# Kernel tuning notes

Hardware: AMD Instinct MI355X
Metric: run time of the kernel (lower is better)

Reference implementation:

```python
import jax, jax.numpy as jnp
from jax import lax
import numpy as np

GRID = 8
H384 = 6 * GRID * GRID  # 384, LSTM input and hidden size


def _conv(x, w, b):
    # x: [B,C,H,W], w: [O,I,kh,kw]
    y = lax.conv_general_dilated(x, w, (1, 1), 'VALID',
                                 dimension_numbers=('NCHW', 'OIHW', 'NCHW'))
    return y + b[None, :, None, None]


def _maxpool2(x):
    return lax.reduce_window(x, -jnp.inf, lax.max,
                             (1, 1, 2, 2), (1, 1, 2, 2), 'VALID')


def setup_inputs() -> dict:
    key = jax.random.key(0)
    ks = jax.random.split(key, 20)
    s = 0.05
    d = {
        'x': jax.random.normal(ks[0], (512, 100, 100), jnp.float32),
        # conv stack: Conv2d(1,16,7) ... Conv2d(128,128,3)
        'cw1': jax.random.normal(ks[1], (16, 1, 7, 7), jnp.float32) * s,
        'cb1': jnp.zeros((16,), jnp.float32),
        'cw2': jax.random.normal(ks[2], (32, 16, 4, 4), jnp.float32) * s,
        'cb2': jnp.zeros((32,), jnp.float32),
        'cw3': jax.random.normal(ks[3], (64, 32, 5, 5), jnp.float32) * s,
        'cb3': jnp.zeros((64,), jnp.float32),
        'cw4': jax.random.normal(ks[4], (128, 64, 5, 5), jnp.float32) * s,
        'cb4': jnp.zeros((128,), jnp.float32),
        'cw5': jax.random.normal(ks[5], (128, 128, 5, 5), jnp.float32) * s,
        'cb5': jnp.zeros((128,), jnp.float32),
        'cw6': jax.random.normal(ks[6], (128, 128, 3, 3), jnp.float32) * s,
        'cb6': jnp.zeros((128,), jnp.float32),
        # linear layers: 8192 -> 1024 -> 384, Sigmoid
        'lw1': jax.random.normal(ks[7], (1024, 8192), jnp.float32) * 0.01,
        'lb1': jnp.zeros((1024,), jnp.float32),
        'lw2': jax.random.normal(ks[8], (384, 1024), jnp.float32) * 0.02,
        'lb2': jnp.zeros((384,), jnp.float32),
        # LSTM (input 384, hidden 384, 1 layer), torch gate order i,f,g,o
        'w_ih': jax.random.normal(ks[9], (4 * H384, H384), jnp.float32) * s,
        'w_hh': jax.random.normal(ks[10], (4 * H384, H384), jnp.float32) * s,
        'b_ih': jnp.zeros((4 * H384,), jnp.float32),
        'b_hh': jnp.zeros((4 * H384,), jnp.float32),
    }
    return d


def reference(x, cw1, cb1, cw2, cb2, cw3, cb3, cw4, cb4, cw5, cb5, cw6, cb6,
              lw1, lb1, lw2, lb2, w_ih, w_hh, b_ih, b_hh):
    B = x.shape[0]
    h = x[:, None, :, :]                       # [B,1,100,100]
    h = _maxpool2(jax.nn.relu(_conv(h, cw1, cb1)))   # [B,16,47,47]
    h = _maxpool2(jax.nn.relu(_conv(h, cw2, cb2)))   # [B,32,22,22]
    h = jax.nn.relu(_conv(h, cw3, cb3))              # [B,64,18,18]
    h = jax.nn.relu(_conv(h, cw4, cb4))              # [B,128,14,14]
    h = jax.nn.relu(_conv(h, cw5, cb5))              # [B,128,10,10]
    h = jax.nn.relu(_conv(h, cw6, cb6))              # [B,128,8,8]
    h = h.reshape(B, -1)                             # [B,8192]
    h = h @ lw1.T + lb1                              # [B,1024]
    h = jax.nn.sigmoid(h @ lw2.T + lb2)              # [B,384]

    # Sequential LSTM over the batch dim with carried (h,c) state
    def step(carry, xt):
        hs, cs = carry
        gates = w_ih @ xt + b_ih + w_hh @ hs + b_hh  # [1536]
        i, f, g, o = jnp.split(gates, 4)
        cs = jax.nn.sigmoid(f) * cs + jax.nn.sigmoid(i) * jnp.tanh(g)
        hs = jax.nn.sigmoid(o) * jnp.tanh(cs)
        return (hs, cs), hs

    init = (jnp.zeros((H384,), x.dtype), jnp.zeros((H384,), x.dtype))
    _, ys = lax.scan(step, init, h)                  # [B,384]
    return ys.reshape(B, 6, GRID, GRID)
```

## Files before the change

### kernel.cpp

```cpp
#include <hip/hip_runtime.h>
#include <cstddef>
#include <cstdint>

#define T256 256

typedef __attribute__((ext_vector_type(8))) short bhalf8;
typedef __attribute__((ext_vector_type(4))) float floatx4;

__device__ __forceinline__ ushort f2bf(float f) {
  union { float f; uint32_t u; } v; v.f = f;
  return (ushort)((v.u + 0x7fffu + ((v.u >> 16) & 1u)) >> 16);
}

__global__ __launch_bounds__(256) void conv1_pool_k(
    const float* __restrict__ x, const float* __restrict__ w,
    const float* __restrict__ bias, float* __restrict__ out)
{
  __shared__ float img[10000];
  __shared__ float wsm[16 * 49];
  __shared__ float bsm[16];
  const int b = blockIdx.x, tid = threadIdx.x;
  for (int i = tid; i < 10000; i += T256) img[i] = x[(size_t)b * 10000 + i];
  for (int i = tid; i < 16 * 49; i += T256) wsm[i] = w[i];
  if (tid < 16) bsm[tid] = bias[tid];
  __syncthreads();
  for (int p = tid; p < 47 * 47; p += T256) {
    const int py = p / 47, px = p % 47;
    const int iy0 = 2 * py, ix0 = 2 * px;
    float win[8][8];
#pragma unroll
    for (int r = 0; r < 8; ++r)
#pragma unroll
      for (int c = 0; c < 8; ++c)
        win[r][c] = img[(iy0 + r) * 100 + (ix0 + c)];
#pragma unroll 2
    for (int oc = 0; oc < 16; ++oc) {
      float m = 0.f;
#pragma unroll
      for (int dy = 0; dy < 2; ++dy)
#pragma unroll
        for (int dx = 0; dx < 2; ++dx) {
          float s = bsm[oc];
#pragma unroll
          for (int ky = 0; ky < 7; ++ky)
#pragma unroll
            for (int kx = 0; kx < 7; ++kx)
              s += win[dy + ky][dx + kx] * wsm[oc * 49 + ky * 7 + kx];
          m = fmaxf(m, s);
        }
      out[((size_t)b * 16 + oc) * 2209 + p] = m;
    }
  }
}

__global__ __launch_bounds__(256) void wprep_k(
    const float* __restrict__ w, ushort* __restrict__ bswz,
    int IC, int KW, int OC, int total)
{
  const int idx = blockIdx.x * 256 + threadIdx.x;
  if (idx >= total) return;
  const int NT = OC / 16;
  const int lane = idx & 63;
  const int nt = (idx >> 6) % NT;
  const int ks = idx / (64 * NT);
  const int oc = nt * 16 + (lane & 15);
  const int kb = ks * 32 + (lane >> 4) * 8;
  ushort tmp[8];
#pragma unroll
  for (int j = 0; j < 8; ++j) {
    const int k = kb + j;
    const int ic = k % IC, tap = k / IC;
    tmp[j] = f2bf(w[((size_t)oc * IC + ic) * (KW * KW) + tap]);
  }
  *(bhalf8*)(bswz + (size_t)idx * 8) = *(const bhalf8*)tmp;
}

__global__ __launch_bounds__(256) void wprep_lin_k(
    const float* __restrict__ w, ushort* __restrict__ bswz,
    int Kdim, int NT, int total)
{
  const int idx = blockIdx.x * 256 + threadIdx.x;
  if (idx >= total) return;
  const int lane = idx & 63;
  const int nt = (idx >> 6) % NT;
  const int ks = idx / (64 * NT);
  const int oc = nt * 16 + (lane & 15);
  const int kb = ks * 32 + (lane >> 4) * 8;
  ushort tmp[8];
#pragma unroll
  for (int j = 0; j < 8; ++j) tmp[j] = f2bf(w[(size_t)oc * Kdim + kb + j]);
  *(bhalf8*)(bswz + (size_t)idx * 8) = *(const bhalf8*)tmp;
}

__global__ __launch_bounds__(256) void f2bf_k(
    const float* __restrict__ in, ushort* __restrict__ outv, int n)
{
  const int i = (blockIdx.x * 256 + threadIdx.x) * 4;
  if (i >= n) return;
  const float4 v = *(const float4*)&in[i];
  ushort tmp[4] = {f2bf(v.x), f2bf(v.y), f2bf(v.z), f2bf(v.w)};
  *(uint2*)&outv[i] = *(const uint2*)tmp;
}

__global__ __launch_bounds__(256) void conv2mfma_k(
    const float* __restrict__ in, const ushort* __restrict__ bswz,
    const float* __restrict__ bias, float* __restrict__ out)
{
  constexpr int IC = 16, IH = 47, IW = 47;
  constexpr int NPIX = IH * IW;
  constexpr int ROWU = IC + 8;
  constexpr int KS = 8;
  __shared__ ushort imgT[NPIX * ROWU];
  const int b = blockIdx.x, tid = threadIdx.x;
  const int lane = tid & 63, wv = tid >> 6;

  for (int e = tid; e < IC * NPIX; e += 256) {
    const int ic = e / NPIX, pix = e % NPIX;
    imgT[pix * ROWU + ic] = f2bf(in[((size_t)b * IC + ic) * NPIX + pix]);
  }
  __syncthreads();

  const int col = lane & 15, g = lane >> 4;
  const float b0 = bias[col], b1 = bias[16 + col];

  for (int it = wv; it < 66; it += 4) {
    const int pyp = it / 3, tx = it - pyp * 3;
    int px = tx * 16 + col; px = px < 43 ? px : 43;
    floatx4 acc[2][2];
#pragma unroll
    for (int dy = 0; dy < 2; ++dy)
#pragma unroll
      for (int nt = 0; nt < 2; ++nt) acc[dy][nt] = (floatx4){0.f, 0.f, 0.f, 0.f};

    for (int ks = 0; ks < KS; ++ks) {
      bhalf8 bf[2];
#pragma unroll
      for (int nt = 0; nt < 2; ++nt)
        bf[nt] = *(const bhalf8*)(bswz + ((size_t)(ks * 2 + nt) * 64 + lane) * 8);
      const int kk = ks * 32 + g * 8;
      const int tap = kk >> 4, icb = kk & 15;
      const int ky = tap >> 2, kx = tap & 3;
      bhalf8 af[2];
#pragma unroll
      for (int dy = 0; dy < 2; ++dy)
        af[dy] = *(const bhalf8*)&imgT[((2 * pyp + dy + ky) * IW + px + kx) * ROWU + icb];
#pragma unroll
      for (int dy = 0; dy < 2; ++dy)
#pragma unroll
        for (int nt = 0; nt < 2; ++nt)
          acc[dy][nt] = __builtin_amdgcn_mfma_f32_16x16x32_bf16(
              af[dy], bf[nt], acc[dy][nt], 0, 0, 0);
    }
#pragma unroll
    for (int nt = 0; nt < 2; ++nt) {
      const int oc = nt * 16 + col;
      const float bb = nt ? b1 : b0;
      float vv[4];
#pragma unroll
      for (int i = 0; i < 4; ++i) vv[i] = fmaxf(acc[0][nt][i], acc[1][nt][i]);
#pragma unroll
      for (int q = 0; q < 2; ++q) {
        const int pxp = tx * 8 + g * 2 + q;
        if (pxp < 22) {
          const float v = fmaxf(fmaxf(vv[2 * q], vv[2 * q + 1]) + bb, 0.f);
          out[((size_t)b * 32 + oc) * 484 + pyp * 22 + pxp] = v;
        }
      }
    }
  }
}

template <int IC, int IH, int IW, int KW_, int OC, int MC>
__global__ __launch_bounds__(256) void convmfma_k(
    const float* __restrict__ in, const ushort* __restrict__ bswz,
    const float* __restrict__ bias, float* __restrict__ out)
{
  constexpr int OH = IH - KW_ + 1, OW = IW - KW_ + 1, P = OH * OW;
  constexpr int NPIX = IH * IW;
  constexpr int KS = IC * KW_ * KW_ / 32;
  constexpr int NT = OC / 16;
  constexpr int NPW = NT / 4;
  constexpr int MT = (P + 15) / 16;
  constexpr int ROWU = IC + 8;
  static_assert(NT % 4 == 0 && IC % 32 == 0, "cfg");

  __shared__ ushort imgT[NPIX * ROWU];
  const int b = blockIdx.x, tid = threadIdx.x;
  const int lane = tid & 63, wv = tid >> 6;
  const int icoff = (lane >> 4) * 8;

  for (int e = tid; e < IC * NPIX; e += 256) {
    const int ic = e / NPIX, pix = e % NPIX;
    imgT[pix * ROWU + ic] = f2bf(in[((size_t)b * IC + ic) * NPIX + pix]);
  }
  __syncthreads();

  for (int m0 = 0; m0 < MT; m0 += MC) {
    floatx4 acc[MC][NPW];
#pragma unroll
    for (int mi = 0; mi < MC; ++mi)
#pragma unroll
      for (int nn = 0; nn < NPW; ++nn)
        acc[mi][nn] = (floatx4){0.f, 0.f, 0.f, 0.f};

    int pbase[MC];
#pragma unroll
    for (int mi = 0; mi < MC; ++mi) {
      int p = (m0 + mi) * 16 + (lane & 15);
      p = p < P ? p : P - 1;
      pbase[mi] = ((p / OW) * IW + (p % OW)) * ROWU;
    }

    bhalf8 bcur[NPW];
#pragma unroll
    for (int nn = 0; nn < NPW; ++nn)
      bcur[nn] = *(const bhalf8*)(bswz + ((size_t)(wv * NPW + nn) * 64 + lane) * 8);

    for (int ks = 0; ks < KS; ++ks) {
      bhalf8 bnext[NPW];
      if (ks + 1 < KS) {
#pragma unroll
        for (int nn = 0; nn < NPW; ++nn)
          bnext[nn] = *(const bhalf8*)(bswz +
              ((size_t)((ks + 1) * NT + wv * NPW + nn) * 64 + lane) * 8);
      }
      const int tap = (ks * 32) / IC;
      const int icb = (ks * 32) % IC;
      const int aoff = ((tap / KW_) * IW + (tap % KW_)) * ROWU + icb + icoff;
      bhalf8 af[MC];
#pragma unroll
      for (int mi = 0; mi < MC; ++mi)
        af[mi] = *(const bhalf8*)&imgT[pbase[mi] + aoff];
#pragma unroll
      for (int mi = 0; mi < MC; ++mi)
#pragma unroll
        for (int nn = 0; nn < NPW; ++nn)
          acc[mi][nn] = __builtin_amdgcn_mfma_f32_16x16x32_bf16(
              af[mi], bcur[nn], acc[mi][nn], 0, 0, 0);
      if (ks + 1 < KS) {
#pragma unroll
        for (int nn = 0; nn < NPW; ++nn) bcur[nn] = bnext[nn];
      }
    }
#pragma unroll
    for (int mi = 0; mi < MC; ++mi)
#pragma unroll
      for (int nn = 0; nn < NPW; ++nn) {
        const int oc = (wv * NPW + nn) * 16 + (lane & 15);
#pragma unroll
        for (int i = 0; i < 4; ++i) {
          const int p = (m0 + mi) * 16 + (lane >> 4) * 4 + i;
          if (p < P) {
            const float v = fmaxf(acc[mi][nn][i] + bias[oc], 0.f);
            out[((size_t)b * OC + oc) * P + p] = v;
          }
        }
      }
  }
}

__global__ __launch_bounds__(256) void gemm_bf16_k(
    const ushort* __restrict__ abf, const ushort* __restrict__ bswz,
    const float* __restrict__ bias, float* __restrict__ C,
    int M, int N, int K)
{
  __shared__ ushort As[64][72];
  const int bn = blockIdx.x, bm = blockIdx.y, tid = threadIdx.x;
  const int lane = tid & 63, wv = tid >> 6;
  const int m0 = bm * 64, n0 = bn * 64;
  const int NTg = N / 16;
  const int ntg = bn * 4 + wv;
  floatx4 acc[4];
#pragma unroll
  for (int mt = 0; mt < 4; ++mt) acc[mt] = (floatx4){0.f, 0.f, 0.f, 0.f};

  for (int kc = 0; kc < K / 64; ++kc) {
    __syncthreads();
#pragma unroll
    for (int q = 0; q < 2; ++q) {
      const int id = q * 256 + tid;
      const int row = id >> 3, kcol = (id & 7) * 8;
      *(bhalf8*)&As[row][kcol] =
          *(const bhalf8*)&abf[(size_t)(m0 + row) * K + kc * 64 + kcol];
    }
    __syncthreads();
#pragma unroll
    for (int k2 = 0; k2 < 2; ++k2) {
      const int ks = kc * 2 + k2;
      const bhalf8 bf = *(const bhalf8*)(bswz + ((size_t)(ks * NTg + ntg) * 64 + lane) * 8);
      const int ksub = k2 * 32 + (lane >> 4) * 8;
#pragma unroll
      for (int mt = 0; mt < 4; ++mt) {
        const bhalf8 af = *(const bhalf8*)&As[mt * 16 + (lane & 15)][ksub];
        acc[mt] = __builtin_amdgcn_mfma_f32_16x16x32_bf16(af, bf, acc[mt], 0, 0, 0);
      }
    }
  }
  const int n = n0 + wv * 16 + (lane & 15);
  const float bb = bias[n];
#pragma unroll
  for (int mt = 0; mt < 4; ++mt)
#pragma unroll
    for (int i = 0; i < 4; ++i) {
      const int m = m0 + mt * 16 + (lane >> 4) * 4 + i;
      C[(size_t)m * N + n] = acc[mt][i] + bb;
    }
}

template <int ACT>
__global__ __launch_bounds__(256) void gemm_tn_k(
    const float* __restrict__ A, const float* __restrict__ B,
    const float* __restrict__ b1, const float* __restrict__ b2,
    float* __restrict__ C, int M, int N, int K)
{
  __shared__ float As[32][66];
  __shared__ float Bs[32][36];
  const int bn = blockIdx.x, bm = blockIdx.y, tid = threadIdx.x;
  const int tx = tid & 7, ty = tid >> 3;
  const int m0 = bm * 64, n0 = bn * 32;
  double acc[2][4] = {{0, 0, 0, 0}, {0, 0, 0, 0}};
  for (int k0 = 0; k0 < K; k0 += 32) {
    __syncthreads();
#pragma unroll
    for (int l = 0; l < 8; ++l) {
      int id = tid + l * 256;
      int kk = id & 31, mm = id >> 5;
      As[kk][mm] = A[(size_t)(m0 + mm) * K + (k0 + kk)];
    }
#pragma unroll
    for (int l = 0; l < 4; ++l) {
      int id = tid + l * 256;
      int kk = id & 31, nn = id >> 5;
      Bs[kk][nn] = B[(size_t)(n0 + nn) * K + (k0 + kk)];
    }
    __syncthreads();
    float p[2][4] = {{0.f, 0.f, 0.f, 0.f}, {0.f, 0.f, 0.f, 0.f}};
#pragma unroll
    for (int kk = 0; kk < 32; ++kk) {
      const float2 av = *reinterpret_cast<const float2*>(&As[kk][ty * 2]);
      const float4 bv = *reinterpret_cast<const float4*>(&Bs[kk][tx * 4]);
      p[0][0] += av.x * bv.x; p[0][1] += av.x * bv.y;
      p[0][2] += av.x * bv.z; p[0][3] += av.x * bv.w;
      p[1][0] += av.y * bv.x; p[1][1] += av.y * bv.y;
      p[1][2] += av.y * bv.z; p[1][3] += av.y * bv.w;
    }
#pragma unroll
    for (int i = 0; i < 2; ++i)
#pragma unroll
      for (int j = 0; j < 4; ++j) acc[i][j] += (double)p[i][j];
  }
#pragma unroll
  for (int i = 0; i < 2; ++i) {
    const int m = m0 + ty * 2 + i;
#pragma unroll
    for (int j = 0; j < 4; ++j) {
      const int n = n0 + tx * 4 + j;
      double v = acc[i][j] + (double)b1[n];
      if (b2) v += (double)b2[n];
      if (ACT == 1) v = 1.0 / (1.0 + exp(-v));
      C[(size_t)m * N + n] = (float)v;
    }
  }
}

#define NWG 16
#define CPW 24
__global__ __launch_bounds__(768) void lstm_k(
    const float* __restrict__ gin, const float* __restrict__ whh,
    float* __restrict__ out, unsigned long long* __restrict__ tagged)
{
  __shared__ __align__(16) float hsm[8][52];
  __shared__ float gsum[96];
  const int wg = blockIdx.x, tid = threadIdx.x;
  const int r = tid >> 3, lk = tid & 7;
  const int gq = r / CPW, cl = r % CPW;
  const int grow = gq * 384 + wg * CPW + cl;
  float wreg[48];
  {
    const float* wr = whh + (size_t)grow * 384 + lk * 48;
#pragma unroll
    for (int i = 0; i < 48; ++i) wreg[i] = wr[i];
  }
  float c = 0.f;
  __syncthreads();
  for (int t = 0; t < 512; ++t) {
    float g0 = 0.f, g1 = 0.f, g2 = 0.f, g3 = 0.f;
    if (tid < CPW) {
      const int j = wg * CPW + tid;
      g0 = gin[(size_t)t * 1536 + 0 * 384 + j];
      g1 = gin[(size_t)t * 1536 + 1 * 384 + j];
      g2 = gin[(size_t)t * 1536 + 2 * 384 + j];
      g3 = gin[(size_t)t * 1536 + 3 * 384 + j];
    }
    if (tid < 384) {
      float hv;
      if (t == 0) {
        hv = 0.f;
      } else {
        unsigned long long u;
        do {
          u = __hip_atomic_load(&tagged[(size_t)(t - 1) * 384 + tid],
                                __ATOMIC_RELAXED, __HIP_MEMORY_SCOPE_AGENT);
        } while ((unsigned)(u >> 32) != (unsigned)t);
        union { unsigned ui; float f; } cv; cv.ui = (unsigned)u; hv = cv.f;
      }
      hsm[tid / 48][tid % 48] = hv;
    }
    __syncthreads();
    float s = 0.f;
    {
      const float4* hp = (const float4*)&hsm[lk][0];
#pragma unroll
      for (int q = 0; q < 12; ++q) {
        const float4 hv = hp[q];
        s += wreg[4 * q + 0] * hv.x + wreg[4 * q + 1] * hv.y
           + wreg[4 * q + 2] * hv.z + wreg[4 * q + 3] * hv.w;
      }
    }
    s += __shfl_xor(s, 1);
    s += __shfl_xor(s, 2);
    s += __shfl_xor(s, 4);
    if (lk == 0) gsum[r] = s;
    __syncthreads();
    if (tid < CPW) {
      const float gi = gsum[0 * CPW + tid] + g0;
      const float gf = gsum[1 * CPW + tid] + g1;
      const float gg = gsum[2 * CPW + tid] + g2;
      const float go = gsum[3 * CPW + tid] + g3;
      const float si = 1.f / (1.f + expf(-gi));
      const float sf = 1.f / (1.f + expf(-gf));
      const float so = 1.f / (1.f + expf(-go));
      c = sf * c + si * tanhf(gg);
      const float hn = so * tanhf(c);
      const int j = wg * CPW + tid;
      union { float f; unsigned ui; } cv; cv.f = hn;
      const unsigned long long pk = ((unsigned long long)(t + 1) << 32) | cv.ui;
      __hip_atomic_store(&tagged[(size_t)t * 384 + j], pk,
                         __ATOMIC_RELAXED, __HIP_MEMORY_SCOPE_AGENT);
      out[(size_t)t * 384 + j] = hn;
    }
  }
}

extern "C" void kernel_launch(void* const* d_in, const int* in_sizes, int n_in,
                              void* d_out, int out_size, void* d_ws, size_t ws_size,
                              hipStream_t stream)
{
  const float* x   = (const float*)d_in[0];
  const float* cw1 = (const float*)d_in[1];
  const float* cb1 = (const float*)d_in[2];
  const float* cw2 = (const float*)d_in[3];
  const float* cb2 = (const float*)d_in[4];
  const float* cw3 = (const float*)d_in[5];
  const float* cb3 = (const float*)d_in[6];
  const float* cw4 = (const float*)d_in[7];
  const float* cb4 = (const float*)d_in[8];
  const float* cw5 = (const float*)d_in[9];
  const float* cb5 = (const float*)d_in[10];
  const float* cw6 = (const float*)d_in[11];
  const float* cb6 = (const float*)d_in[12];
  const float* lw1 = (const float*)d_in[13];
  const float* lb1 = (const float*)d_in[14];
  const float* lw2 = (const float*)d_in[15];
  const float* lb2 = (const float*)d_in[16];
  const float* wih = (const float*)d_in[17];
  const float* whh = (const float*)d_in[18];
  const float* bih = (const float*)d_in[19];
  const float* bhh = (const float*)d_in[20];
  float* out = (float*)d_out;
  char* ws = (char*)d_ws;

  float* bufA = (float*)(ws);
  float* bufB = (float*)(ws + 72384512);
  float* l1o  = (float*)(ws + 123764736);
  float* x2   = (float*)(ws + 125861888);
  float* gin  = (float*)(ws + 126648320);
  ushort* bw3 = (ushort*)(ws + 123764736);
  ushort* bw4 = (ushort*)(ws + 123764736 + 102400);
  ushort* bw5 = (ushort*)(ws + 123764736 + 512000);
  ushort* bw6 = (ushort*)(ws + 123764736 + 1331200);
  ushort* bw2 = (ushort*)(ws + 123764736 + 1626112);
  ushort* bw1 = (ushort*)(ws);
  ushort* abf = (ushort*)(ws + 16777216);
  unsigned long long* tagged = (unsigned long long*)(ws + 25165824);

  wprep_k<<<(25 * 4 * 64 + 255) / 256, 256, 0, stream>>>(cw3, bw3, 32, 5, 64, 25 * 4 * 64);
  wprep_k<<<(50 * 8 * 64 + 255) / 256, 256, 0, stream>>>(cw4, bw4, 64, 5, 128, 50 * 8 * 64);
  wprep_k<<<(100 * 8 * 64 + 255) / 256, 256, 0, stream>>>(cw5, bw5, 128, 5, 128, 100 * 8 * 64);
  wprep_k<<<(36 * 8 * 64 + 255) / 256, 256, 0, stream>>>(cw6, bw6, 128, 3, 128, 36 * 8 * 64);
  wprep_k<<<(8 * 2 * 64 + 255) / 256, 256, 0, stream>>>(cw2, bw2, 16, 4, 32, 8 * 2 * 64);

  conv1_pool_k<<<512, 256, 0, stream>>>(x, cw1, cb1, bufA);
  conv2mfma_k<<<512, 256, 0, stream>>>(bufA, bw2, cb2, bufB);
  convmfma_k<32, 22, 22, 5, 64, 7><<<512, 256, 0, stream>>>(bufB, bw3, cb3, bufA);
  convmfma_k<64, 18, 18, 5, 128, 7><<<512, 256, 0, stream>>>(bufA, bw4, cb4, bufB);
  convmfma_k<128, 14, 14, 5, 128, 7><<<512, 256, 0, stream>>>(bufB, bw5, cb5, bufA);
  convmfma_k<128, 10, 10, 3, 128, 4><<<512, 256, 0, stream>>>(bufA, bw6, cb6, bufB);
  wprep_lin_k<<<(256 * 64 * 64 + 255) / 256, 256, 0, stream>>>(lw1, bw1, 8192, 64, 256 * 64 * 64);
  f2bf_k<<<(512 * 8192 / 4 + 255) / 256, 256, 0, stream>>>(bufB, abf, 512 * 8192);
  hipMemsetAsync(tagged, 0, 512 * 384 * 8, stream);
  gemm_bf16_k<<<dim3(16, 8), 256, 0, stream>>>(abf, bw1, lb1, l1o, 512, 1024, 8192);
  gemm_tn_k<1><<<dim3(384 / 32, 512 / 64), 256, 0, stream>>>(l1o, lw2, lb2, nullptr, x2, 512, 384, 1024);
  gemm_tn_k<0><<<dim3(1536 / 32, 512 / 64), 256, 0, stream>>>(x2, wih, bih, bhh, gin, 512, 1536, 384);
  lstm_k<<<NWG, 768, 0, stream>>>(gin, whh, out, tagged);
}
```

Baseline: 1.597 ms.

## Remove LSTM per-step barrier via in-wave gate reduction and double-buffered h

The LSTM kernel now maps each wave to two hidden columns with all four gates inside the wave. Gate sums are combined with shuffles instead of shared memory, which removes the second __syncthreads per timestep. The h buffer is double-buffered in shared memory so the remaining barrier is enough to separate reads from the next writes. Separately, conv1 loads each output channel's 49 weights into registers with unroll 1, which may raise register pressure but cuts repeated LDS reads.

```diff
diff --git a/kernel.cpp b/kernel.cpp
--- a/kernel.cpp
+++ b/kernel.cpp
@@ -33,8 +33,11 @@
 #pragma unroll
       for (int c = 0; c < 8; ++c)
         win[r][c] = img[(iy0 + r) * 100 + (ix0 + c)];
-#pragma unroll 2
+#pragma unroll 1
     for (int oc = 0; oc < 16; ++oc) {
+      float wr[49];
+#pragma unroll
+      for (int j = 0; j < 49; ++j) wr[j] = wsm[oc * 49 + j];
       float m = 0.f;
 #pragma unroll
       for (int dy = 0; dy < 2; ++dy)
@@ -45,7 +48,7 @@
           for (int ky = 0; ky < 7; ++ky)
 #pragma unroll
             for (int kx = 0; kx < 7; ++kx)
-              s += win[dy + ky][dx + kx] * wsm[oc * 49 + ky * 7 + kx];
+              s += win[dy + ky][dx + kx] * wr[ky * 7 + kx];
           m = fmaxf(m, s);
         }
       out[((size_t)b * 16 + oc) * 2209 + p] = m;
@@ -369,29 +372,22 @@
     const float* __restrict__ gin, const float* __restrict__ whh,
     float* __restrict__ out, unsigned long long* __restrict__ tagged)
 {
-  __shared__ __align__(16) float hsm[8][52];
-  __shared__ float gsum[96];
+  __shared__ __align__(16) float hsm[2][8][52];
   const int wg = blockIdx.x, tid = threadIdx.x;
-  const int r = tid >> 3, lk = tid & 7;
-  const int gq = r / CPW, cl = r % CPW;
-  const int grow = gq * 384 + wg * CPW + cl;
+  const int w = tid >> 6, l = tid & 63;
+  const int ch = l >> 5, gate = (l >> 3) & 3, sub = l & 7;
+  const int col = wg * CPW + w * 2 + ch;
   float wreg[48];
   {
-    const float* wr = whh + (size_t)grow * 384 + lk * 48;
+    const float* wr = whh + ((size_t)gate * 384 + col) * 384 + sub * 48;
 #pragma unroll
     for (int i = 0; i < 48; ++i) wreg[i] = wr[i];
   }
   float c = 0.f;
   __syncthreads();
   for (int t = 0; t < 512; ++t) {
-    float g0 = 0.f, g1 = 0.f, g2 = 0.f, g3 = 0.f;
-    if (tid < CPW) {
-      const int j = wg * CPW + tid;
-      g0 = gin[(size_t)t * 1536 + 0 * 384 + j];
-      g1 = gin[(size_t)t * 1536 + 1 * 384 + j];
-      g2 = gin[(size_t)t * 1536 + 2 * 384 + j];
-      g3 = gin[(size_t)t * 1536 + 3 * 384 + j];
-    }
+    float ginv = 0.f;
+    if (sub == 0) ginv = gin[(size_t)t * 1536 + gate * 384 + col];
     if (tid < 384) {
       float hv;
       if (t == 0) {
@@ -404,12 +400,12 @@
         } while ((unsigned)(u >> 32) != (unsigned)t);
         union { unsigned ui; float f; } cv; cv.ui = (unsigned)u; hv = cv.f;
       }
-      hsm[tid / 48][tid % 48] = hv;
+      hsm[t & 1][tid / 48][tid % 48] = hv;
     }
     __syncthreads();
     float s = 0.f;
     {
-      const float4* hp = (const float4*)&hsm[lk][0];
+      const float4* hp = (const float4*)&hsm[t & 1][sub][0];
 #pragma unroll
       for (int q = 0; q < 12; ++q) {
         const float4 hv = hp[q];
@@ -420,24 +416,23 @@
     s += __shfl_xor(s, 1);
     s += __shfl_xor(s, 2);
     s += __shfl_xor(s, 4);
-    if (lk == 0) gsum[r] = s;
-    __syncthreads();
-    if (tid < CPW) {
-      const float gi = gsum[0 * CPW + tid] + g0;
-      const float gf = gsum[1 * CPW + tid] + g1;
-      const float gg = gsum[2 * CPW + tid] + g2;
-      const float go = gsum[3 * CPW + tid] + g3;
+    const float sg = s + ginv;
+    const int base = l & 32;
+    const float gi = __shfl(sg, base);
+    const float gf = __shfl(sg, base + 8);
+    const float gg = __shfl(sg, base + 16);
+    const float go = __shfl(sg, base + 24);
+    if ((l & 31) == 0) {
       const float si = 1.f / (1.f + expf(-gi));
       const float sf = 1.f / (1.f + expf(-gf));
       const float so = 1.f / (1.f + expf(-go));
       c = sf * c + si * tanhf(gg);
       const float hn = so * tanhf(c);
-      const int j = wg * CPW + tid;
       union { float f; unsigned ui; } cv; cv.f = hn;
       const unsigned long long pk = ((unsigned long long)(t + 1) << 32) | cv.ui;
-      __hip_atomic_store(&tagged[(size_t)t * 384 + j], pk,
+      __hip_atomic_store(&tagged[(size_t)t * 384 + col], pk,
                          __ATOMIC_RELAXED, __HIP_MEMORY_SCOPE_AGENT);
-      out[(size_t)t * 384 + j] = hn;
+      out[(size_t)t * 384 + col] = hn;
     }
   }
 }
```

Measured after the change: 1.968 ms. +23.2%, slower.
